# Kernel tuning notes

Measured on AMD Instinct MI355X. Metric: run time of the kernel, lower is better.

Reference implementation:

```python
import jax, jax.numpy as jnp
import numpy as np

N_NODES, N_EDGES, H, Q, RBF = 10000, 160000, 128, 16, 32
CUTOFF_UPPER = 4.5


def tensor_norm(t):
    # Frobenius norm squared over the trailing 3x3 dims -> [n, h]
    return (t * t).sum((-2, -1))


def decompose_tensor(X):
    # X: [n, h, 3, 3] -> I: [n, h] (trace/3), A skew, S symmetric-traceless
    eye = jnp.eye(3, dtype=X.dtype)
    I = jnp.einsum('nhii->nh', X) / 3.0
    Xt = jnp.swapaxes(X, -1, -2)
    A = 0.5 * (X - Xt)
    S = 0.5 * (X + Xt) - I[..., None, None] * eye
    return I, A, S


def I_to_tensor(I):
    return I[..., None, None] * jnp.eye(3, dtype=I.dtype)


def skewtensor_to_vector(A):
    return jnp.stack((A[..., 2, 1], A[..., 0, 2], A[..., 1, 0]), axis=-1)


def vector_to_skewtensor(v):
    z = jnp.zeros_like(v[..., 0])
    rows = jnp.stack((z, -v[..., 2], v[..., 1],
                      v[..., 2], z, -v[..., 0],
                      -v[..., 1], v[..., 0], z), axis=-1)
    return rows.reshape(v.shape[:-1] + (3, 3))


def setup_inputs() -> dict:
    key = jax.random.key(0)
    ks = jax.random.split(key, 12)
    d_in = RBF + 2 * Q  # 64
    inp = {
        'X': jax.random.normal(ks[0], (N_NODES, H, 3, 3), jnp.float32),
        'charges': jax.random.normal(ks[1], (N_NODES, Q), jnp.float32),
        'edge_weight': jax.random.uniform(ks[2], (N_EDGES,), jnp.float32) * CUTOFF_UPPER,
        'edge_attr': jax.random.normal(ks[3], (N_EDGES, RBF), jnp.float32),
        'W1': jax.random.normal(ks[4], (d_in, H), jnp.float32) / np.sqrt(d_in),
        'b1': jnp.zeros((H,), jnp.float32),
        'W2': jax.random.normal(ks[5], (H, 2 * H), jnp.float32) / np.sqrt(H),
        'b2': jnp.zeros((2 * H,), jnp.float32),
        'W3': jax.random.normal(ks[6], (2 * H, 3 * H), jnp.float32) / np.sqrt(2 * H),
        'b3': jnp.zeros((3 * H,), jnp.float32),
        'Wt': jax.random.normal(ks[7], (6, H, H), jnp.float32) / np.sqrt(H),
        'edge_index': jax.random.randint(ks[8], (2, N_EDGES), 0, N_NODES, jnp.int64 if jax.config.jax_enable_x64 else jnp.int32),
    }
    return inp


def reference(X, charges, edge_weight, edge_attr, W1, b1, W2, b2, W3, b3, Wt, edge_index):
    n, h = X.shape[0], X.shape[1]
    src, dst = edge_index[0], edge_index[1]

    # CosineCutoff (cutoff_lower = 0)
    C = 0.5 * (jnp.cos(edge_weight * (jnp.pi / CUTOFF_UPPER)) + 1.0)
    C = C * (edge_weight < CUTOFF_UPPER).astype(X.dtype)

    # edge MLP on [edge_attr | charges_i | charges_j]
    x = jnp.concatenate([edge_attr, charges[src], charges[dst]], axis=-1)
    x = jax.nn.silu(x @ W1 + b1)
    x = jax.nn.silu(x @ W2 + b2)
    x = jax.nn.silu(x @ W3 + b3)
    x = (x * C[:, None]).reshape(-1, 3, h)  # [E, 3, h]

    # normalize node tensor features
    X = X / (tensor_norm(X) + 1.0)[..., None, None]
    I, A, S = decompose_tensor(X)
    I = I @ Wt[0]
    A = jnp.einsum('nhij,hg->ngij', A, Wt[1])
    S = jnp.einsum('nhij,hg->ngij', S, Wt[2])
    Y = A + S + I_to_tensor(I)

    # message passing: gather from dst node, scale by edge factor, scatter-add to src
    Im = jax.ops.segment_sum(x[:, 0, :] * I[dst], src, num_segments=n)
    Av = skewtensor_to_vector(A)
    Am_vec = jax.ops.segment_sum(x[:, 1, :, None] * Av[dst], src, num_segments=n)
    Sm = jax.ops.segment_sum(x[:, 2, :, None, None] * S[dst], src, num_segments=n)
    msg = vector_to_skewtensor(Am_vec) + Sm + I_to_tensor(Im)

    # O(3) recombination
    A2 = jnp.matmul(msg, Y)
    B2 = jnp.matmul(Y, msg)
    I, A, S = decompose_tensor(A2 + B2)

    _X = A + S + I_to_tensor(I)
    normp1 = tensor_norm(_X) + 1.0
    I = I / normp1
    A = A / normp1[..., None, None]
    S = S / normp1[..., None, None]
    I = I @ Wt[3]
    A = jnp.einsum('nhij,hg->ngij', A, Wt[4])
    S = jnp.einsum('nhij,hg->ngij', S, Wt[5])
    dX = A + S + I_to_tensor(I)

    return X + dX + jnp.matmul(dX, dX)
```

## Files before the change

### kernel.cpp

```cpp
#include <hip/hip_runtime.h>
#include <math.h>

#define NND 10000
#define NE  160000
#define HD  128
#define NH  (NND*HD)

typedef _Float16 f16;
typedef _Float16 half8 __attribute__((ext_vector_type(8)));
typedef _Float16 half4 __attribute__((ext_vector_type(4)));
typedef float floatx4 __attribute__((ext_vector_type(4)));

__device__ __forceinline__ float silu_f(float v) {
    return v * (1.0f / (1.0f + __expf(-v)));
}

__global__ __launch_bounds__(256) void w_prep(const float* __restrict__ W1,
                                              const float* __restrict__ W2,
                                              const float* __restrict__ W3,
                                              const float* __restrict__ Wt,
                                              f16* __restrict__ w1t,
                                              f16* __restrict__ w2t,
                                              f16* __restrict__ w3t,
                                              f16* __restrict__ wtT) {
    int id = blockIdx.x * 256 + threadIdx.x;
    if (id < 128*64) { int n = id >> 6, k = id & 63;  w1t[id] = (f16)W1[k*128 + n]; return; }
    id -= 128*64;
    if (id < 256*128) { int n = id >> 7, k = id & 127; w2t[id] = (f16)W2[k*256 + n]; return; }
    id -= 256*128;
    if (id < 384*256) { int n = id >> 8, k = id & 255; w3t[id] = (f16)W3[k*384 + n]; return; }
    id -= 384*256;
    if (id < 6*128*128) {
        int wi = id >> 14, rem = id & 16383;
        int n = rem >> 7, k = rem & 127;
        wtT[(size_t)wi*16384 + n*128 + k] = (f16)Wt[(size_t)wi*16384 + k*128 + n];
    }
}

__global__ __launch_bounds__(256) void hist_kernel(const int* __restrict__ eidx,
                                                   int* __restrict__ hist) {
    int e = blockIdx.x * 256 + threadIdx.x;
    if (e < NE) atomicAdd(&hist[eidx[e]], 1);
}

__global__ __launch_bounds__(1024) void scan_kernel(const int* __restrict__ hist,
                                                    int* __restrict__ offs,
                                                    int* __restrict__ cursor) {
    __shared__ int sums[1024];
    int t = threadIdx.x;
    int base = t * 10;
    int loc[10]; int s = 0;
    #pragma unroll
    for (int i = 0; i < 10; i++) {
        int v = (base + i < NND) ? hist[base + i] : 0;
        loc[i] = s; s += v;
    }
    sums[t] = s;
    __syncthreads();
    for (int off = 1; off < 1024; off <<= 1) {
        int v = (t >= off) ? sums[t - off] : 0;
        __syncthreads();
        sums[t] += v;
        __syncthreads();
    }
    int basesum = (t > 0) ? sums[t - 1] : 0;
    #pragma unroll
    for (int i = 0; i < 10; i++)
        if (base + i < NND) { offs[base + i] = basesum + loc[i]; cursor[base + i] = basesum + loc[i]; }
}

__global__ __launch_bounds__(256) void scatter_kernel(const int* __restrict__ eidx,
                                                      int* __restrict__ cursor,
                                                      int* __restrict__ perm,
                                                      int* __restrict__ ssrc,
                                                      int* __restrict__ sdst) {
    int e = blockIdx.x * 256 + threadIdx.x;
    if (e >= NE) return;
    int s = eidx[e], d = eidx[NE + e];
    int pos = atomicAdd(&cursor[s], 1);
    perm[pos] = e; ssrc[pos] = s; sdst[pos] = d;
}

__global__ __launch_bounds__(256) void node_prep(const float* __restrict__ X,
                                                 f16* __restrict__ comp) {
    int idx = blockIdx.x * 256 + threadIdx.x;
    if (idx >= NH) return;
    const float* xp = X + (size_t)idx * 9;
    float x[9];
    #pragma unroll
    for (int i = 0; i < 9; i++) x[i] = xp[i];
    float nsq = 0.f;
    #pragma unroll
    for (int i = 0; i < 9; i++) nsq = fmaf(x[i], x[i], nsq);
    float inv = 1.0f / (nsq + 1.0f);
    #pragma unroll
    for (int i = 0; i < 9; i++) x[i] *= inv;

    float I0  = (x[0] + x[4] + x[8]) * (1.0f / 3.0f);
    float a0  = 0.5f * (x[7] - x[5]);
    float a1  = 0.5f * (x[2] - x[6]);
    float a2  = 0.5f * (x[3] - x[1]);
    float s00 = x[0] - I0;
    float s11 = x[4] - I0;
    float s22 = x[8] - I0;
    float s01 = 0.5f * (x[1] + x[3]);
    float s02 = 0.5f * (x[2] + x[6]);
    float s12 = 0.5f * (x[5] + x[7]);

    comp[0*NH + idx] = (f16)I0;
    comp[1*NH + idx] = (f16)a0;  comp[2*NH + idx] = (f16)a1;  comp[3*NH + idx] = (f16)a2;
    comp[4*NH + idx] = (f16)s00; comp[5*NH + idx] = (f16)s11; comp[6*NH + idx] = (f16)s22;
    comp[7*NH + idx] = (f16)s01; comp[8*NH + idx] = (f16)s02; comp[9*NH + idx] = (f16)s12;
}

__global__ __launch_bounds__(256) void mix_mfma(const f16* __restrict__ A,
                                                const f16* __restrict__ WtT,
                                                float* __restrict__ C,
                                                f16* __restrict__ Ch,
                                                int w0, int w1, int w2,
                                                int writeC, int writeCh) {
    const int g = blockIdx.y;
    const int baseRow = (g == 0) ? 0   : (g == 1 ? NND   : 4*NND);
    const int Mg      = (g == 0) ? NND : (g == 1 ? 3*NND : 6*NND);
    const int row0 = blockIdx.x * 64;
    if (row0 >= Mg) return;
    const int wi = (g == 0) ? w0 : (g == 1 ? w1 : w2);
    const f16* B = WtT + (size_t)wi * 128 * 128;

    __shared__ f16 As[64 * 136];

    const int t = threadIdx.x;
    const int l = t & 63, wid = t >> 6, lr = l & 15, lh = l >> 4;

    #pragma unroll
    for (int i = 0; i < 4; i++) {
        int id = t + 256 * i;
        int r = id >> 4, ch = id & 15;
        int rr = row0 + r; if (rr >= Mg) rr = Mg - 1;
        *(half8*)&As[r*136 + ch*8] =
            *(const half8*)&A[((size_t)baseRow + rr) * HD + ch*8];
    }
    __syncthreads();

    floatx4 acc[8];
    #pragma unroll
    for (int n = 0; n < 8; n++) acc[n] = (floatx4)0.0f;

    #pragma unroll
    for (int k0 = 0; k0 < 128; k0 += 32) {
        half8 a = *(const half8*)&As[(wid*16 + lr)*136 + k0 + lh*8];
        #pragma unroll
        for (int n = 0; n < 8; n++) {
            half8 b = *(const half8*)&B[(size_t)(n*16 + lr)*128 + k0 + lh*8];
            acc[n] = __builtin_amdgcn_mfma_f32_16x16x32_f16(a, b, acc[n], 0, 0, 0);
        }
    }

    #pragma unroll
    for (int n = 0; n < 8; n++) {
        #pragma unroll
        for (int r = 0; r < 4; r++) {
            int gl = row0 + wid*16 + lh*4 + r;
            if (gl < Mg) {
                size_t grow = (size_t)baseRow + gl;
                int col = n*16 + lr;
                float val = acc[n][r];
                if (writeC) C[grow * HD + col] = val;
                if (writeCh) {
                    int plane = (int)(grow / NND);
                    int node  = (int)(grow - (size_t)plane * NND);
                    Ch[((size_t)node * 10 + plane) * HD + col] = (f16)val;
                }
            }
        }
    }
}

__global__ __launch_bounds__(256, 4) void edge_gemm12(
    const float* __restrict__ edge_attr, const float* __restrict__ charges,
    const int* __restrict__ offs,
    const int* __restrict__ perm, const int* __restrict__ ssrc, const int* __restrict__ sdst,
    const f16* __restrict__ W1t, const float* __restrict__ b1,
    const f16* __restrict__ W2t, const float* __restrict__ b2,
    f16* __restrict__ x2b, int n0, int n1)
{
    __shared__ __align__(16) char pool[33280];
    f16* x0s  = (f16*)pool;
    f16* x1s  = (f16*)(pool + 9216);
    f16* x2st = (f16*)pool;
    __shared__ int srcS[64], dstS[64], permS[64];

    const int pbase = offs[n0];
    const int pend  = (n1 >= NND) ? NE : offs[n1];
    const int eb    = blockIdx.x * 64;
    if (pbase + eb >= pend) return;

    const int t = threadIdx.x;
    const int l = t & 63, wid = t >> 6, lr = l & 15, lh = l >> 4;

    if (t < 64) {
        int pe = pbase + eb + t;
        if (pe > NE - 1) pe = NE - 1;
        permS[t] = perm[pe];
        srcS[t]  = ssrc[pe];
        dstS[t]  = sdst[pe];
    }
    __syncthreads();

    {
        int e = t >> 2, q = t & 3;
        #pragma unroll
        for (int jj = 0; jj < 2; jj++) {
            int j = q + jj*4;
            float4 va = *(const float4*)&edge_attr[(size_t)permS[e]*32 + j*4];
            half4 hv; hv[0]=(f16)va.x; hv[1]=(f16)va.y; hv[2]=(f16)va.z; hv[3]=(f16)va.w;
            *(half4*)&x0s[e*72 + j*4] = hv;
        }
        int node = (q < 2) ? srcS[e] : dstS[e];
        int qq   = (q < 2) ? q : (q - 2);
        int cb   = (q < 2) ? 32 : 48;
        #pragma unroll
        for (int jj = 0; jj < 2; jj++) {
            int j = qq + jj*2;
            float4 vc = *(const float4*)&charges[(size_t)node*16 + j*4];
            half4 hv; hv[0]=(f16)vc.x; hv[1]=(f16)vc.y; hv[2]=(f16)vc.z; hv[3]=(f16)vc.w;
            *(half4*)&x0s[e*72 + cb + j*4] = hv;
        }
    }
    __syncthreads();

    {
        floatx4 acc[2][4];
        #pragma unroll
        for (int n = 0; n < 2; n++)
            #pragma unroll
            for (int m = 0; m < 4; m++) acc[n][m] = (floatx4)0.0f;

        #pragma unroll
        for (int k0 = 0; k0 < 64; k0 += 32) {
            half8 a[4];
            #pragma unroll
            for (int m = 0; m < 4; m++)
                a[m] = *(const half8*)&x0s[(m*16 + lr)*72 + k0 + lh*8];
            #pragma unroll
            for (int n = 0; n < 2; n++) {
                half8 b = *(const half8*)&W1t[(size_t)(wid*32 + n*16 + lr)*64 + k0 + lh*8];
                #pragma unroll
                for (int m = 0; m < 4; m++)
                    acc[n][m] = __builtin_amdgcn_mfma_f32_16x16x32_f16(a[m], b, acc[n][m], 0, 0, 0);
            }
        }
        #pragma unroll
        for (int n = 0; n < 2; n++) {
            int col = wid*32 + n*16 + lr;
            float bb = b1[col];
            #pragma unroll
            for (int m = 0; m < 4; m++)
                #pragma unroll
                for (int r = 0; r < 4; r++)
                    x1s[(m*16 + lh*4 + r)*140 + col] = (f16)silu_f(acc[n][m][r] + bb);
        }
    }
    __syncthreads();

    {
        floatx4 acc[4][4];
        #pragma unroll
        for (int n = 0; n < 4; n++)
            #pragma unroll
            for (int m = 0; m < 4; m++) acc[n][m] = (floatx4)0.0f;

        #pragma unroll
        for (int k0 = 0; k0 < 128; k0 += 32) {
            half8 a[4];
            #pragma unroll
            for (int m = 0; m < 4; m++)
                a[m] = *(const half8*)&x1s[(m*16 + lr)*140 + k0 + lh*8];
            #pragma unroll
            for (int n = 0; n < 4; n++) {
                half8 b = *(const half8*)&W2t[(size_t)(wid*64 + n*16 + lr)*128 + k0 + lh*8];
                #pragma unroll
                for (int m = 0; m < 4; m++)
                    acc[n][m] = __builtin_amdgcn_mfma_f32_16x16x32_f16(a[m], b, acc[n][m], 0, 0, 0);
            }
        }
        __syncthreads();
        #pragma unroll
        for (int n = 0; n < 4; n++) {
            int col = wid*64 + n*16 + lr;
            float bb = b2[col];
            #pragma unroll
            for (int m = 0; m < 4; m++)
                #pragma unroll
                for (int r = 0; r < 4; r++)
                    x2st[(m*16 + lh*4 + r)*260 + col] = (f16)silu_f(acc[n][m][r] + bb);
        }
    }
    __syncthreads();

    #pragma unroll
    for (int i = 0; i < 8; i++) {
        int c = t + 256 * i;
        int e = c >> 5, j = c & 31;
        *(half8*)&x2b[(size_t)(eb + e)*256 + j*8] = *(const half8*)&x2st[e*260 + j*8];
    }
}

__global__ __launch_bounds__(256, 3) void edge_gemm3(
    const float* __restrict__ edge_weight,
    const int* __restrict__ offs, const int* __restrict__ perm,
    const f16* __restrict__ x2b,
    const f16* __restrict__ W3t, const float* __restrict__ b3,
    f16* __restrict__ vbuf, int n0, int n1)
{
    __shared__ __align__(16) char pool[49664];
    f16* As    = (f16*)pool;
    f16* stage = (f16*)pool;
    __shared__ float Cs[64];

    const int pbase = offs[n0];
    const int pend  = (n1 >= NND) ? NE : offs[n1];
    const int eb    = blockIdx.x * 64;
    if (pbase + eb >= pend) return;

    const int t = threadIdx.x;
    const int l = t & 63, wid = t >> 6, lr = l & 15, lh = l >> 4;

    if (t < 64) {
        int pe = pbase + eb + t;
        if (pe > NE - 1) pe = NE - 1;
        float w = edge_weight[perm[pe]];
        float c = 0.5f * (cosf(w * (float)(M_PI / 4.5)) + 1.0f);
        Cs[t] = (w < 4.5f) ? c : 0.0f;
    }

    floatx4 acc[6][4];
    #pragma unroll
    for (int n = 0; n < 6; n++)
        #pragma unroll
        for (int m = 0; m < 4; m++) acc[n][m] = (floatx4)0.0f;

    #pragma unroll
    for (int kb = 0; kb < 2; kb++) {
        __syncthreads();
        #pragma unroll
        for (int i = 0; i < 4; i++) {
            int id = t + 256 * i;
            int r = id >> 4, c = id & 15;
            *(half8*)&As[r*136 + c*8] =
                *(const half8*)&x2b[(size_t)(eb + r)*256 + kb*128 + c*8];
        }
        __syncthreads();

        #pragma unroll
        for (int k0 = 0; k0 < 128; k0 += 32) {
            half8 a[4];
            #pragma unroll
            for (int m = 0; m < 4; m++)
                a[m] = *(const half8*)&As[(m*16 + lr)*136 + k0 + lh*8];
            #pragma unroll
            for (int n = 0; n < 6; n++) {
                half8 b = *(const half8*)&W3t[(size_t)(wid*96 + n*16 + lr)*256 + kb*128 + k0 + lh*8];
                #pragma unroll
                for (int m = 0; m < 4; m++)
                    acc[n][m] = __builtin_amdgcn_mfma_f32_16x16x32_f16(a[m], b, acc[n][m], 0, 0, 0);
            }
        }
    }
    __syncthreads();

    #pragma unroll
    for (int n = 0; n < 6; n++) {
        int col = wid*96 + n*16 + lr;
        float bb = b3[col];
        #pragma unroll
        for (int m = 0; m < 4; m++)
            #pragma unroll
            for (int r = 0; r < 4; r++) {
                int e = m*16 + lh*4 + r;
                stage[e*388 + col] = (f16)(silu_f(acc[n][m][r] + bb) * Cs[e]);
            }
    }
    __syncthreads();

    #pragma unroll
    for (int i = 0; i < 12; i++) {
        int c = t + 256 * i;
        int e = c / 48, j = c - e * 48;
        *(half8*)&vbuf[(size_t)(eb + e)*384 + j*8] = *(const half8*)&stage[e*388 + j*8];
    }
}

__global__ __launch_bounds__(128) void scatter_combine(
    const int* __restrict__ offs, const int* __restrict__ ends,
    const int* __restrict__ sdst, const f16* __restrict__ vbuf,
    const f16* __restrict__ Ych,
    f16* __restrict__ pre, int n0, int VC)
{
    const int s = n0 + blockIdx.x;
    const int h = threadIdx.x;
    const int pbase = offs[n0];
    const int p0 = offs[s], p1 = ends[s];

    float ps[10];
    #pragma unroll
    for (int c = 0; c < 10; c++) ps[c] = 0.f;

    int p = p0;
    for (; p + 1 < p1; p += 2) {
        int sl0 = p - pbase, sl1 = sl0 + 1;
        int d0 = sdst[p], d1 = sdst[p + 1];
        const f16* y0 = Ych + (size_t)d0 * 1280 + h;
        const f16* y1 = Ych + (size_t)d1 * 1280 + h;
        float va0 = (float)vbuf[(size_t)sl0*384 + h];
        float vb0 = (float)vbuf[(size_t)sl0*384 + 128 + h];
        float vc0 = (float)vbuf[(size_t)sl0*384 + 256 + h];
        float va1 = (float)vbuf[(size_t)sl1*384 + h];
        float vb1 = (float)vbuf[(size_t)sl1*384 + 128 + h];
        float vc1 = (float)vbuf[(size_t)sl1*384 + 256 + h];
        float y0r[10], y1r[10];
        #pragma unroll
        for (int c = 0; c < 10; c++) { y0r[c] = (float)y0[c*HD]; y1r[c] = (float)y1[c*HD]; }
        ps[0] = fmaf(va0, y0r[0], ps[0]);
        #pragma unroll
        for (int c = 1; c < 4; c++)  ps[c] = fmaf(vb0, y0r[c], ps[c]);
        #pragma unroll
        for (int c = 4; c < 10; c++) ps[c] = fmaf(vc0, y0r[c], ps[c]);
        ps[0] = fmaf(va1, y1r[0], ps[0]);
        #pragma unroll
        for (int c = 1; c < 4; c++)  ps[c] = fmaf(vb1, y1r[c], ps[c]);
        #pragma unroll
        for (int c = 4; c < 10; c++) ps[c] = fmaf(vc1, y1r[c], ps[c]);
    }
    if (p < p1) {
        int sl0 = p - pbase;
        int d0 = sdst[p];
        const f16* y0 = Ych + (size_t)d0 * 1280 + h;
        float va0 = (float)vbuf[(size_t)sl0*384 + h];
        float vb0 = (float)vbuf[(size_t)sl0*384 + 128 + h];
        float vc0 = (float)vbuf[(size_t)sl0*384 + 256 + h];
        float y0r[10];
        #pragma unroll
        for (int c = 0; c < 10; c++) y0r[c] = (float)y0[c*HD];
        ps[0] = fmaf(va0, y0r[0], ps[0]);
        #pragma unroll
        for (int c = 1; c < 4; c++)  ps[c] = fmaf(vb0, y0r[c], ps[c]);
        #pragma unroll
        for (int c = 4; c < 10; c++) ps[c] = fmaf(vc0, y0r[c], ps[c]);
    }

    const f16* ys = Ych + (size_t)s * 1280 + h;
    float yI  = (float)ys[0*HD];
    float ya0 = (float)ys[1*HD], ya1 = (float)ys[2*HD], ya2 = (float)ys[3*HD];
    float ys00 = (float)ys[4*HD], ys11 = (float)ys[5*HD], ys22 = (float)ys[6*HD];
    float ys01 = (float)ys[7*HD], ys02 = (float)ys[8*HD], ys12 = (float)ys[9*HD];

    float M[3][3] = {
        { ps[0] + ps[4],  ps[7] - ps[3],  ps[8] + ps[2] },
        { ps[7] + ps[3],  ps[0] + ps[5],  ps[9] - ps[1] },
        { ps[8] - ps[2],  ps[9] + ps[1],  ps[0] + ps[6] } };
    float Y[3][3] = {
        { yI + ys00,  ys01 - ya2, ys02 + ya1 },
        { ys01 + ya2, yI + ys11,  ys12 - ya0 },
        { ys02 - ya1, ys12 + ya0, yI + ys22  } };

    float T[3][3];
    #pragma unroll
    for (int r = 0; r < 3; r++)
        #pragma unroll
        for (int c = 0; c < 3; c++) {
            float acc = 0.f;
            #pragma unroll
            for (int k = 0; k < 3; k++)
                acc += M[r][k] * Y[k][c] + Y[r][k] * M[k][c];
            T[r][c] = acc;
        }

    float tr3 = (T[0][0] + T[1][1] + T[2][2]) * (1.0f / 3.0f);
    float nsq = 0.f;
    #pragma unroll
    for (int r = 0; r < 3; r++)
        #pragma unroll
        for (int c = 0; c < 3; c++) nsq = fmaf(T[r][c], T[r][c], nsq);
    float inv = 1.0f / (nsq + 1.0f);

    const size_t idx = (size_t)s * HD + h;
    pre[0*(size_t)NH + idx] = (f16)(tr3 * inv);
    pre[1*(size_t)NH + idx] = (f16)(0.5f * (T[2][1] - T[1][2]) * inv);
    pre[2*(size_t)NH + idx] = (f16)(0.5f * (T[0][2] - T[2][0]) * inv);
    pre[3*(size_t)NH + idx] = (f16)(0.5f * (T[1][0] - T[0][1]) * inv);
    pre[4*(size_t)NH + idx] = (f16)((T[0][0] - tr3) * inv);
    pre[5*(size_t)NH + idx] = (f16)((T[1][1] - tr3) * inv);
    pre[6*(size_t)NH + idx] = (f16)((T[2][2] - tr3) * inv);
    pre[7*(size_t)NH + idx] = (f16)(0.5f * (T[0][1] + T[1][0]) * inv);
    pre[8*(size_t)NH + idx] = (f16)(0.5f * (T[0][2] + T[2][0]) * inv);
    pre[9*(size_t)NH + idx] = (f16)(0.5f * (T[1][2] + T[2][1]) * inv);
}

__global__ __launch_bounds__(256) void final_out(const float* __restrict__ post,
                                                 const float* __restrict__ X,
                                                 float* __restrict__ out) {
    int idx = blockIdx.x * 256 + threadIdx.x;
    if (idx >= NH) return;

    float dI  = post[0*NH + idx];
    float da0 = post[1*NH + idx], da1 = post[2*NH + idx], da2 = post[3*NH + idx];
    float ds00 = post[4*NH + idx], ds11 = post[5*NH + idx], ds22 = post[6*NH + idx];
    float ds01 = post[7*NH + idx], ds02 = post[8*NH + idx], ds12 = post[9*NH + idx];

    float D[3][3] = {
        { dI + ds00,  ds01 - da2, ds02 + da1 },
        { ds01 + da2, dI + ds11,  ds12 - da0 },
        { ds02 - da1, ds12 + da0, dI + ds22  } };

    const float* xp = X + (size_t)idx * 9;
    float x[9];
    #pragma unroll
    for (int i = 0; i < 9; i++) x[i] = xp[i];
    float nsq = 0.f;
    #pragma unroll
    for (int i = 0; i < 9; i++) nsq = fmaf(x[i], x[i], nsq);
    float inv = 1.0f / (nsq + 1.0f);

    float* op = out + (size_t)idx * 9;
    #pragma unroll
    for (int r = 0; r < 3; r++)
        #pragma unroll
        for (int c = 0; c < 3; c++) {
            float p = 0.f;
            #pragma unroll
            for (int k = 0; k < 3; k++) p = fmaf(D[r][k], D[k][c], p);
            op[r*3 + c] = x[r*3 + c] * inv + D[r][c] + p;
        }
}

extern "C" void kernel_launch(void* const* d_in, const int* in_sizes, int n_in,
                              void* d_out, int out_size, void* d_ws, size_t ws_size,
                              hipStream_t stream) {
    const float* X       = (const float*)d_in[0];
    const float* charges = (const float*)d_in[1];
    const float* ew      = (const float*)d_in[2];
    const float* ea      = (const float*)d_in[3];
    const float* W1      = (const float*)d_in[4];
    const float* b1      = (const float*)d_in[5];
    const float* W2      = (const float*)d_in[6];
    const float* b2      = (const float*)d_in[7];
    const float* W3      = (const float*)d_in[8];
    const float* b3      = (const float*)d_in[9];
    const float* Wt      = (const float*)d_in[10];
    const int*   eidx    = (const int*)d_in[11];
    float* out = (float*)d_out;

    float* f32a  = (float*)d_ws;
    f16*   fh16  = (f16*)(f32a + (size_t)10 * NH);
    f16*   ych   = fh16 + (size_t)10 * NH;
    f16*   w1t   = ych + (size_t)10 * NH;
    f16*   w2t   = w1t + 128*64;
    f16*   w3t   = w2t + 256*128;
    f16*   wtT   = w3t + 384*256;
    int*   hist   = (int*)(wtT + 6*128*128);
    int*   offs   = hist + NND;
    int*   cursor = offs + NND;
    int*   perm   = cursor + NND;
    int*   ssrc   = perm + NE;
    int*   sdst   = ssrc + NE;
    f16*   vbuf   = (f16*)(sdst + NE);

    size_t used = (size_t)((char*)vbuf - (char*)d_ws);
    int Q, VC;
    if      (used + (size_t)160000 * 1280 <= ws_size) { Q = 1; VC = 160000; }
    else if (used + (size_t) 84480 * 1280 <= ws_size) { Q = 2; VC = 84480;  }
    else if (used + (size_t) 48000 * 1280 <= ws_size) { Q = 4; VC = 48000;  }
    else                                              { Q = 8; VC = 24320;  }
    f16* x2b = vbuf + (size_t)VC * 384;

    hipMemsetAsync(hist, 0, NND * sizeof(int), stream);

    w_prep<<<928, 256, 0, stream>>>(W1, W2, W3, Wt, w1t, w2t, w3t, wtT);
    node_prep<<<NH / 256, 256, 0, stream>>>(X, fh16);

    hist_kernel<<<(NE + 255) / 256, 256, 0, stream>>>(eidx, hist);
    scan_kernel<<<1, 1024, 0, stream>>>(hist, offs, cursor);
    scatter_kernel<<<(NE + 255) / 256, 256, 0, stream>>>(eidx, cursor, perm, ssrc, sdst);

    dim3 gmix((6 * NND + 63) / 64, 3);
    mix_mfma<<<gmix, 256, 0, stream>>>(fh16, wtT, f32a, ych, 0, 1, 2, 0, 1);

    const int nodesPer = NND / Q;
    for (int q = 0; q < Q; q++) {
        int n0 = q * nodesPer, n1 = n0 + nodesPer;
        int nb = VC / 64;
        edge_gemm12<<<nb, 256, 0, stream>>>(ea, charges, offs, perm, ssrc, sdst,
                                            w1t, b1, w2t, b2, x2b, n0, n1);
        edge_gemm3<<<nb, 256, 0, stream>>>(ew, offs, perm, x2b, w3t, b3,
                                           vbuf, n0, n1);
        scatter_combine<<<nodesPer, 128, 0, stream>>>(offs, cursor, sdst, vbuf,
                                                      ych, fh16, n0, VC);
    }

    mix_mfma<<<gmix, 256, 0, stream>>>(fh16, wtT, f32a, ych, 3, 4, 5, 1, 0);

    final_out<<<NH / 256, 256, 0, stream>>>(f32a, X, out);
}
```

Before: 435.7 us.

## Halve edge GEMM epilogue LDS staging and store post-mix output in fp16

The edge_gemm12 and edge_gemm3 epilogues now stage output in two 32-row phases, which shrinks their shared-memory pools so more blocks fit per CU (launch bounds raised to 5 and 6). The second mix_mfma pass writes fp16 plane-major output instead of fp32, and final_out reads fp16, halving that intermediate's traffic. The trade-offs are extra barriers per phase, possible register spilling under the tighter launch bounds, and lower precision in the final correction term.

```diff
diff --git a/kernel.cpp b/kernel.cpp
--- a/kernel.cpp
+++ b/kernel.cpp
@@ -115,10 +115,10 @@
 
 __global__ __launch_bounds__(256) void mix_mfma(const f16* __restrict__ A,
                                                 const f16* __restrict__ WtT,
-                                                float* __restrict__ C,
-                                                f16* __restrict__ Ch,
+                                                f16* __restrict__ Cn,
+                                                f16* __restrict__ Cp,
                                                 int w0, int w1, int w2,
-                                                int writeC, int writeCh) {
+                                                int writeNode, int writePlane) {
     const int g = blockIdx.y;
     const int baseRow = (g == 0) ? 0   : (g == 1 ? NND   : 4*NND);
     const int Mg      = (g == 0) ? NND : (g == 1 ? 3*NND : 6*NND);
@@ -165,18 +165,18 @@
                 size_t grow = (size_t)baseRow + gl;
                 int col = n*16 + lr;
                 float val = acc[n][r];
-                if (writeC) C[grow * HD + col] = val;
-                if (writeCh) {
+                if (writePlane) Cp[grow * HD + col] = (f16)val;
+                if (writeNode) {
                     int plane = (int)(grow / NND);
                     int node  = (int)(grow - (size_t)plane * NND);
-                    Ch[((size_t)node * 10 + plane) * HD + col] = (f16)val;
+                    Cn[((size_t)node * 10 + plane) * HD + col] = (f16)val;
                 }
             }
         }
     }
 }
 
-__global__ __launch_bounds__(256, 4) void edge_gemm12(
+__global__ __launch_bounds__(256, 5) void edge_gemm12(
     const float* __restrict__ edge_attr, const float* __restrict__ charges,
     const int* __restrict__ offs,
     const int* __restrict__ perm, const int* __restrict__ ssrc, const int* __restrict__ sdst,
@@ -184,7 +184,7 @@
     const f16* __restrict__ W2t, const float* __restrict__ b2,
     f16* __restrict__ x2b, int n0, int n1)
 {
-    __shared__ __align__(16) char pool[33280];
+    __shared__ __align__(16) char pool[27136];
     f16* x0s  = (f16*)pool;
     f16* x1s  = (f16*)(pool + 9216);
     f16* x2st = (f16*)pool;
@@ -285,35 +285,42 @@
             }
         }
         __syncthreads();
-        #pragma unroll
-        for (int n = 0; n < 4; n++) {
-            int col = wid*64 + n*16 + lr;
-            float bb = b2[col];
-            #pragma unroll
-            for (int m = 0; m < 4; m++)
+
+        #pragma unroll
+        for (int ph = 0; ph < 2; ph++) {
+            #pragma unroll
+            for (int n = 0; n < 4; n++) {
+                int col = wid*64 + n*16 + lr;
+                float bb = b2[col];
                 #pragma unroll
-                for (int r = 0; r < 4; r++)
-                    x2st[(m*16 + lh*4 + r)*260 + col] = (f16)silu_f(acc[n][m][r] + bb);
-        }
-    }
-    __syncthreads();
-
-    #pragma unroll
-    for (int i = 0; i < 8; i++) {
-        int c = t + 256 * i;
-        int e = c >> 5, j = c & 31;
-        *(half8*)&x2b[(size_t)(eb + e)*256 + j*8] = *(const half8*)&x2st[e*260 + j*8];
-    }
-}
-
-__global__ __launch_bounds__(256, 3) void edge_gemm3(
+                for (int mm = 0; mm < 2; mm++) {
+                    int m = ph*2 + mm;
+                    #pragma unroll
+                    for (int r = 0; r < 4; r++)
+                        x2st[(mm*16 + lh*4 + r)*260 + col] = (f16)silu_f(acc[n][m][r] + bb);
+                }
+            }
+            __syncthreads();
+            #pragma unroll
+            for (int i = 0; i < 4; i++) {
+                int c = t + 256 * i;
+                int e = c >> 5, j = c & 31;
+                *(half8*)&x2b[(size_t)(eb + ph*32 + e)*256 + j*8] =
+                    *(const half8*)&x2st[e*260 + j*8];
+            }
+            __syncthreads();
+        }
+    }
+}
+
+__global__ __launch_bounds__(256, 6) void edge_gemm3(
     const float* __restrict__ edge_weight,
     const int* __restrict__ offs, const int* __restrict__ perm,
     const f16* __restrict__ x2b,
     const f16* __restrict__ W3t, const float* __restrict__ b3,
     f16* __restrict__ vbuf, int n0, int n1)
 {
-    __shared__ __align__(16) char pool[49664];
+    __shared__ __align__(16) char pool[24832];
     f16* As    = (f16*)pool;
     f16* stage = (f16*)pool;
     __shared__ float Cs[64];
@@ -370,24 +377,31 @@
     __syncthreads();
 
     #pragma unroll
-    for (int n = 0; n < 6; n++) {
-        int col = wid*96 + n*16 + lr;
-        float bb = b3[col];
-        #pragma unroll
-        for (int m = 0; m < 4; m++)
-            #pragma unroll
-            for (int r = 0; r < 4; r++) {
-                int e = m*16 + lh*4 + r;
-                stage[e*388 + col] = (f16)(silu_f(acc[n][m][r] + bb) * Cs[e]);
+    for (int ph = 0; ph < 2; ph++) {
+        #pragma unroll
+        for (int n = 0; n < 6; n++) {
+            int col = wid*96 + n*16 + lr;
+            float bb = b3[col];
+            #pragma unroll
+            for (int mm = 0; mm < 2; mm++) {
+                int m = ph*2 + mm;
+                #pragma unroll
+                for (int r = 0; r < 4; r++) {
+                    int e  = mm*16 + lh*4 + r;
+                    int ge = m*16 + lh*4 + r;
+                    stage[e*388 + col] = (f16)(silu_f(acc[n][m][r] + bb) * Cs[ge]);
+                }
             }
-    }
-    __syncthreads();
-
-    #pragma unroll
-    for (int i = 0; i < 12; i++) {
-        int c = t + 256 * i;
-        int e = c / 48, j = c - e * 48;
-        *(half8*)&vbuf[(size_t)(eb + e)*384 + j*8] = *(const half8*)&stage[e*388 + j*8];
+        }
+        __syncthreads();
+        #pragma unroll
+        for (int i = 0; i < 6; i++) {
+            int c = t + 256 * i;
+            int e = c / 48, j = c - e * 48;
+            *(half8*)&vbuf[(size_t)(eb + ph*32 + e)*384 + j*8] =
+                *(const half8*)&stage[e*388 + j*8];
+        }
+        __syncthreads();
     }
 }
 
@@ -497,16 +511,16 @@
     pre[9*(size_t)NH + idx] = (f16)(0.5f * (T[1][2] + T[2][1]) * inv);
 }
 
-__global__ __launch_bounds__(256) void final_out(const float* __restrict__ post,
+__global__ __launch_bounds__(256) void final_out(const f16* __restrict__ post,
                                                  const float* __restrict__ X,
                                                  float* __restrict__ out) {
     int idx = blockIdx.x * 256 + threadIdx.x;
     if (idx >= NH) return;
 
-    float dI  = post[0*NH + idx];
-    float da0 = post[1*NH + idx], da1 = post[2*NH + idx], da2 = post[3*NH + idx];
-    float ds00 = post[4*NH + idx], ds11 = post[5*NH + idx], ds22 = post[6*NH + idx];
-    float ds01 = post[7*NH + idx], ds02 = post[8*NH + idx], ds12 = post[9*NH + idx];
+    float dI  = (float)post[0*(size_t)NH + idx];
+    float da0 = (float)post[1*(size_t)NH + idx], da1 = (float)post[2*(size_t)NH + idx], da2 = (float)post[3*(size_t)NH + idx];
+    float ds00 = (float)post[4*(size_t)NH + idx], ds11 = (float)post[5*(size_t)NH + idx], ds22 = (float)post[6*(size_t)NH + idx];
+    float ds01 = (float)post[7*(size_t)NH + idx], ds02 = (float)post[8*(size_t)NH + idx], ds12 = (float)post[9*(size_t)NH + idx];
 
     float D[3][3] = {
         { dI + ds00,  ds01 - da2, ds02 + da1 },
@@ -551,8 +565,8 @@
     const int*   eidx    = (const int*)d_in[11];
     float* out = (float*)d_out;
 
-    float* f32a  = (float*)d_ws;
-    f16*   fh16  = (f16*)(f32a + (size_t)10 * NH);
+    f16*   posth = (f16*)d_ws;
+    f16*   fh16  = posth + (size_t)10 * NH;
     f16*   ych   = fh16 + (size_t)10 * NH;
     f16*   w1t   = ych + (size_t)10 * NH;
     f16*   w2t   = w1t + 128*64;
@@ -584,7 +598,7 @@
     scatter_kernel<<<(NE + 255) / 256, 256, 0, stream>>>(eidx, cursor, perm, ssrc, sdst);
 
     dim3 gmix((6 * NND + 63) / 64, 3);
-    mix_mfma<<<gmix, 256, 0, stream>>>(fh16, wtT, f32a, ych, 0, 1, 2, 0, 1);
+    mix_mfma<<<gmix, 256, 0, stream>>>(fh16, wtT, ych, posth, 0, 1, 2, 1, 0);
 
     const int nodesPer = NND / Q;
     for (int q = 0; q < Q; q++) {
@@ -598,7 +612,7 @@
                                                       ych, fh16, n0, VC);
     }
 
-    mix_mfma<<<gmix, 256, 0, stream>>>(fh16, wtT, f32a, ych, 3, 4, 5, 1, 0);
-
-    final_out<<<NH / 256, 256, 0, stream>>>(f32a, X, out);
-}
+    mix_mfma<<<gmix, 256, 0, stream>>>(fh16, wtT, ych, posth, 3, 4, 5, 0, 1);
+
+    final_out<<<NH / 256, 256, 0, stream>>>(posth, X, out);
+}
```

After: 881.6 us. 102% more time.
